# Optimization experiments

Measured on AMD Instinct MI355X. Metric: run time of the kernel, lower is better.

## Reference

```python
import jax, jax.numpy as jnp
import numpy as np

HIDDEN = 2048
HEADS = 16
HEAD_DIM = HIDDEN // HEADS  # 128
MLA_DIM = max(HEAD_DIM // 4, 8)  # 32
WINDOW = 512
B, S = 4, 2048


def setup_inputs() -> dict:
    key = jax.random.key(0)
    ks = jax.random.split(key, 9)
    sc = 0.02
    return {
        "x": jax.random.normal(ks[0], (B, S, HIDDEN), jnp.float32),
        "wq": jax.random.normal(ks[1], (HIDDEN, HIDDEN), jnp.float32) * sc,
        "wk": jax.random.normal(ks[2], (HEAD_DIM, HIDDEN), jnp.float32) * sc,
        "wv": jax.random.normal(ks[3], (HEAD_DIM, HIDDEN), jnp.float32) * sc,
        "wo": jax.random.normal(ks[4], (HIDDEN, HIDDEN), jnp.float32) * sc,
        "k_compress_w": jax.random.normal(ks[5], (MLA_DIM, HEAD_DIM), jnp.float32) * sc,
        "v_compress_w": jax.random.normal(ks[6], (MLA_DIM, HEAD_DIM), jnp.float32) * sc,
        "k_decompress_w": jax.random.normal(ks[7], (HEAD_DIM, MLA_DIM), jnp.float32) * sc,
        "v_decompress_w": jax.random.normal(ks[8], (HEAD_DIM, MLA_DIM), jnp.float32) * sc,
    }


def _rope_tables(seq_len, dim):
    inv_freq = 1.0 / (10000.0 ** (jnp.arange(0, dim, 2, dtype=jnp.float32) / dim))
    t = jnp.arange(seq_len, dtype=jnp.float32)
    freqs = jnp.outer(t, inv_freq)            # [S, dim/2]
    emb = jnp.concatenate([freqs, freqs], -1)  # [S, dim]
    return jnp.cos(emb), jnp.sin(emb)


def _rotate_half(x):
    h = x.shape[-1] // 2
    return jnp.concatenate([-x[..., h:], x[..., :h]], axis=-1)


def _quant_dequant_8bit(t):
    # global min/max 8-bit fake-quant (round has zero grad, matching uint8 detach)
    t_min, t_max = t.min(), t.max()
    scale = (t_max - t_min) / 255.0
    q = jnp.clip(jnp.round((t - t_min) / scale), 0.0, 255.0)
    return q * scale + t_min


def _swat(scores):
    attn = jax.nn.sigmoid(scores)
    return attn / (attn.sum(axis=-1, keepdims=True) + 1e-8)


def reference(x, wq, wk, wv, wo, k_compress_w, v_compress_w, k_decompress_w, v_decompress_w):
    b, s, _ = x.shape
    scale = 1.0 / np.sqrt(HEAD_DIM)

    Q = (x @ wq.T).reshape(b, s, HEADS, HEAD_DIM).transpose(0, 2, 1, 3)  # [B,H,S,D]
    K = (x @ wk.T)[:, None]  # [B,1,S,D] (single shared KV head, MQA)
    V = (x @ wv.T)[:, None]

    # RoPE (cos/sin broadcast over batch and heads)
    cos, sin = _rope_tables(s, HEAD_DIM)
    Q = Q * cos + _rotate_half(Q) * sin
    K = K * cos + _rotate_half(K) * sin

    # MLA compress -> decompress (low-rank)
    K = (K @ k_compress_w.T) @ k_decompress_w.T
    V = (V @ v_compress_w.T) @ v_decompress_w.T

    # 8-bit fake quantization
    K = _quant_dequant_8bit(K)
    V = _quant_dequant_8bit(V)

    # Sliding-window SWAT attention with linear blending of overlaps
    step = WINDOW // 2
    out = jnp.zeros_like(Q)
    for i in range(0, s, step):
        e = min(i + WINDOW, s)
        Qw = Q[:, :, i:e]           # [B,H,w,D]
        Kw = K[:, :, i:e]           # [B,1,w,D]
        Vw = V[:, :, i:e]
        scores = jnp.matmul(Qw, Kw.swapaxes(-2, -1)) * scale  # [B,H,w,w]
        wout = jnp.matmul(_swat(scores), Vw)                   # [B,H,w,D]
        if i == 0:
            out = out.at[:, :, i:e].set(wout)
        else:
            ov = min(step, e - i)
            alpha = jnp.linspace(0.0, 1.0, ov).reshape(1, 1, -1, 1)
            blended = (1 - alpha) * out[:, :, i:i + ov] + alpha * wout[:, :, :ov]
            out = out.at[:, :, i:i + ov].set(blended)
            if i + ov < e:
                out = out.at[:, :, i + ov:e].set(wout[:, :, ov:])

    out = out.transpose(0, 2, 1, 3).reshape(b, s, HIDDEN)
    return out @ wo.T
```

## Files before the change

### kernel.cpp

```cpp
#include <hip/hip_runtime.h>
#include <hip/hip_bf16.h>
#include <hip/hip_fp16.h>
#include <math.h>

#define BB 4
#define SS 2048
#define HIDDEN 2048
#define NHEADS 16
#define HDIM 128
#define BSROWS (BB * SS)
#define ATT_SCALE 0.08838834764831845f

typedef __attribute__((ext_vector_type(8))) _Float16 half8v;
typedef __attribute__((ext_vector_type(4))) float f32x4;
typedef __attribute__((ext_vector_type(16))) float f32x16;

static __device__ __forceinline__ unsigned encf(float x) {
  unsigned b = __float_as_uint(x);
  return (b & 0x80000000u) ? ~b : (b | 0x80000000u);
}
static __device__ __forceinline__ float decf(unsigned k) {
  unsigned b = (k & 0x80000000u) ? (k ^ 0x80000000u) : ~k;
  return __uint_as_float(b);
}
static __device__ __forceinline__ unsigned short f2h(float f) {
  _Float16 h = (_Float16)f;
  return *(unsigned short*)&h;
}


__global__ void rope_tables_k(float* __restrict__ ct, float* __restrict__ st) {
  int t = blockIdx.x;
  int d = threadIdx.x;
  float inv = powf(10000.0f, -(float)d * (1.0f / 64.0f));
  float a = (float)t * inv;
  ct[t * 64 + d] = cosf(a);
  st[t * 64 + d] = sinf(a);
}

__global__ void build_m_k(const float* __restrict__ kc, const float* __restrict__ kdw,
                          const float* __restrict__ vc, const float* __restrict__ vdw,
                          float* __restrict__ mk, float* __restrict__ mv) {
  int a = blockIdx.x;
  int c = threadIdx.x;
  const float* cw = blockIdx.y ? vc : kc;
  const float* dw = blockIdx.y ? vdw : kdw;
  float* m = blockIdx.y ? mv : mk;
  float acc = 0.f;
#pragma unroll
  for (int mm = 0; mm < 32; mm++) acc += cw[mm * 128 + a] * dw[c * 32 + mm];
  m[a * 128 + c] = acc;
}

__global__ void mm_init_k(unsigned* mmx) {
  int i = threadIdx.x;
  if (i < 4) mmx[i] = (i & 1) ? 0u : 0xFFFFFFFFu;
}

__global__ void split_fp16_k(const float* __restrict__ src,
                             unsigned short* __restrict__ hi, int n4) {
  int i = blockIdx.x * 256 + threadIdx.x;
  int stride = gridDim.x * 256;
  for (; i < n4; i += stride) {
    float4 v = ((const float4*)src)[i];
    ((ushort4*)hi)[i] = make_ushort4(f2h(v.x), f2h(v.y), f2h(v.z), f2h(v.w));
  }
}

__global__ __launch_bounds__(512, 2) void gemm_f16_ph_k(
    const unsigned short* __restrict__ A, const unsigned short* __restrict__ B,
    float* __restrict__ C, int NBX) {
  __shared__ unsigned short As[2][256 * 64];
  __shared__ unsigned short Bs[2][256 * 64];
  const int K = 2048;
  const int nsteps = 32;
  int tid = threadIdx.x;
  int lane = tid & 63;
  int wid = tid >> 6;
  int wm = wid >> 2, wn = wid & 3;
  int l31 = lane & 31, lg2 = lane >> 5;
  int swz = (l31 & 7) << 4;

  int nwg = gridDim.x;
  int cpx = nwg >> 3;
  int sbid = ((int)blockIdx.x & 7) * cpx + ((int)blockIdx.x >> 3);
  int by = sbid / NBX, bx = sbid % NBX;
  int m0 = by * 256, n0 = bx * 256;

  f32x16 acc[4][2] = {};

#define STAGE_A_HALF(tt_, h_, sl_)                                                 \
  do {                                                                             \
    int k0a_ = (tt_) << 6;                                                         \
    _Pragma("unroll") for (int j_ = 0; j_ < 2; ++j_) {                             \
      int L_ = j_ * 8192 + tid * 16;                                               \
      int hr_ = L_ >> 7;                                                           \
      int r_ = (hr_ & 63) + ((hr_ & 64) << 1) + (h_) * 64;                         \
      int cb_ = (L_ & 127) ^ ((r_ & 7) << 4);                                      \
      __builtin_amdgcn_global_load_lds(                                            \
          (const __attribute__((address_space(1))) void*)(A +                      \
              (size_t)(m0 + r_) * K + k0a_ + (cb_ >> 1)),                          \
          (__attribute__((address_space(3))) void*)((char*)&As[sl_][0] +           \
              (h_) * 8192 + j_ * 16384 + tid * 16), 16, 0, 0);                     \
    }                                                                              \
  } while (0)

#define STAGE_B_HALF(tt_, h_, sl_)                                                 \
  do {                                                                             \
    int k0b_ = (tt_) << 6;                                                         \
    _Pragma("unroll") for (int j_ = 0; j_ < 2; ++j_) {                             \
      int L_ = j_ * 8192 + tid * 16;                                               \
      int hr_ = L_ >> 7;                                                           \
      int r_ = (hr_ & 63) + ((hr_ & 64) << 1) + (h_) * 64;                         \
      int cb_ = (L_ & 127) ^ ((r_ & 7) << 4);                                      \
      __builtin_amdgcn_global_load_lds(                                            \
          (const __attribute__((address_space(1))) void*)(B +                      \
              (size_t)(n0 + r_) * K + k0b_ + (cb_ >> 1)),                          \
          (__attribute__((address_space(3))) void*)((char*)&Bs[sl_][0] +           \
              (h_) * 8192 + j_ * 16384 + tid * 16), 16, 0, 0);                     \
    }                                                                              \
  } while (0)

  STAGE_A_HALF(0, 0, 0);
  STAGE_A_HALF(0, 1, 0);
  STAGE_B_HALF(0, 0, 0);
  STAGE_B_HALF(0, 1, 0);
  STAGE_A_HALF(1, 0, 1);
  asm volatile("s_waitcnt vmcnt(2)" ::: "memory");
  __builtin_amdgcn_sched_barrier(0);
  __builtin_amdgcn_s_barrier();

  for (int t = 0; t < nsteps; ++t) {
    int s = t & 1;
    const char* Ab = (const char*)&As[s][0];
    const char* Bb = (const char*)&Bs[s][0];
    half8v afr[2][4], bfr[2][4];
#pragma unroll
    for (int ks = 0; ks < 4; ++ks) {
      int cb = (ks * 32 + lg2 * 16) ^ swz;
      afr[0][ks] = *(const half8v*)(Ab + (wm * 128 + 0 + l31) * 128 + cb);
      afr[1][ks] = *(const half8v*)(Ab + (wm * 128 + 32 + l31) * 128 + cb);
      bfr[0][ks] = *(const half8v*)(Bb + (wn * 64 + 0 + l31) * 128 + cb);
      bfr[1][ks] = *(const half8v*)(Bb + (wn * 64 + 32 + l31) * 128 + cb);
    }
    if (t < nsteps - 1) {
      STAGE_A_HALF(t + 1, 1, s ^ 1);
      STAGE_B_HALF(t + 1, 0, s ^ 1);
      STAGE_B_HALF(t + 1, 1, s ^ 1);
    }
    __builtin_amdgcn_s_barrier();
    asm volatile("s_waitcnt lgkmcnt(0)" ::: "memory");
    __builtin_amdgcn_sched_barrier(0);
    __builtin_amdgcn_s_setprio(1);
#pragma unroll
    for (int ks = 0; ks < 4; ++ks) {
      acc[0][0] = __builtin_amdgcn_mfma_f32_32x32x16_f16(afr[0][ks], bfr[0][ks], acc[0][0], 0, 0, 0);
      acc[0][1] = __builtin_amdgcn_mfma_f32_32x32x16_f16(afr[0][ks], bfr[1][ks], acc[0][1], 0, 0, 0);
      acc[1][0] = __builtin_amdgcn_mfma_f32_32x32x16_f16(afr[1][ks], bfr[0][ks], acc[1][0], 0, 0, 0);
      acc[1][1] = __builtin_amdgcn_mfma_f32_32x32x16_f16(afr[1][ks], bfr[1][ks], acc[1][1], 0, 0, 0);
    }
    __builtin_amdgcn_s_setprio(0);
    __builtin_amdgcn_s_barrier();
#pragma unroll
    for (int ks = 0; ks < 4; ++ks) {
      int cb = (ks * 32 + lg2 * 16) ^ swz;
      afr[0][ks] = *(const half8v*)(Ab + (wm * 128 + 64 + l31) * 128 + cb);
      afr[1][ks] = *(const half8v*)(Ab + (wm * 128 + 96 + l31) * 128 + cb);
    }
    if (t < nsteps - 2)
      STAGE_A_HALF(t + 2, 0, s);
    __builtin_amdgcn_s_barrier();
    asm volatile("s_waitcnt lgkmcnt(0)" ::: "memory");
    __builtin_amdgcn_sched_barrier(0);
    __builtin_amdgcn_s_setprio(1);
#pragma unroll
    for (int ks = 0; ks < 4; ++ks) {
      acc[2][0] = __builtin_amdgcn_mfma_f32_32x32x16_f16(afr[0][ks], bfr[0][ks], acc[2][0], 0, 0, 0);
      acc[2][1] = __builtin_amdgcn_mfma_f32_32x32x16_f16(afr[0][ks], bfr[1][ks], acc[2][1], 0, 0, 0);
      acc[3][0] = __builtin_amdgcn_mfma_f32_32x32x16_f16(afr[1][ks], bfr[0][ks], acc[3][0], 0, 0, 0);
      acc[3][1] = __builtin_amdgcn_mfma_f32_32x32x16_f16(afr[1][ks], bfr[1][ks], acc[3][1], 0, 0, 0);
    }
    __builtin_amdgcn_s_setprio(0);
    if (t < nsteps - 2)
      asm volatile("s_waitcnt vmcnt(2)" ::: "memory");
    else
      asm volatile("s_waitcnt vmcnt(0)" ::: "memory");
    __builtin_amdgcn_sched_barrier(0);
    __builtin_amdgcn_s_barrier();
  }
#undef STAGE_A_HALF
#undef STAGE_B_HALF

#pragma unroll
  for (int mi = 0; mi < 4; ++mi) {
#pragma unroll
    for (int ni = 0; ni < 2; ++ni) {
      int col = n0 + wn * 64 + ni * 32 + l31;
#pragma unroll
      for (int r = 0; r < 16; ++r) {
        int row = m0 + wm * 128 + mi * 32 + (r & 3) + 8 * (r >> 2) + 4 * lg2;
        C[(size_t)row * 2048 + col] = acc[mi][ni][r];
      }
    }
  }
}

__global__ __launch_bounds__(256) void gemm_f16_kv_k(
    const unsigned short* __restrict__ A, const unsigned short* __restrict__ B,
    float* __restrict__ Ckv) {
  const int K = 2048;
  __shared__ unsigned short As[128 * 64];
  __shared__ unsigned short Bs[128 * 64];
  int tid = threadIdx.x;
  int lane = tid & 63, wid = tid >> 6;
  int wr = wid >> 1, wc = wid & 1;
  int m0 = blockIdx.y * 128, n0 = blockIdx.x * 128;

  f32x4 acc[4][4] = {};

  int off_ = (wid << 10) + (lane << 4);
  int l15 = lane & 15, lk = lane >> 4;

  for (int t = 0; t < 32; ++t) {
    int k0 = t << 6;
    __syncthreads();
#pragma unroll
    for (int c = 0; c < 4; ++c) {
      int off = off_ + (c << 12);
      int row = off >> 7;
      int cole = (off & 127) >> 1;
      const unsigned short* ga = A + (size_t)(m0 + row) * K + k0 + cole;
      const unsigned short* gb = B + (size_t)(n0 + row) * K + k0 + cole;
      __builtin_amdgcn_global_load_lds(
          (const __attribute__((address_space(1))) void*)ga,
          (__attribute__((address_space(3))) void*)((char*)As + off), 16, 0, 0);
      __builtin_amdgcn_global_load_lds(
          (const __attribute__((address_space(1))) void*)gb,
          (__attribute__((address_space(3))) void*)((char*)Bs + off), 16, 0, 0);
    }
    __syncthreads();
#pragma unroll
    for (int ks = 0; ks < 2; ++ks) {
      half8v af[4], bf[4];
#pragma unroll
      for (int f = 0; f < 4; ++f) {
        int arow = wr * 64 + f * 16 + l15;
        int brow = wc * 64 + f * 16 + l15;
        int colb = ks * 64 + lk * 16;
        af[f] = *(const half8v*)((const char*)As + arow * 128 + colb);
        bf[f] = *(const half8v*)((const char*)Bs + brow * 128 + colb);
      }
#pragma unroll
      for (int fm = 0; fm < 4; ++fm)
#pragma unroll
        for (int fn = 0; fn < 4; ++fn)
          acc[fm][fn] = __builtin_amdgcn_mfma_f32_16x16x32_f16(af[fm], bf[fn], acc[fm][fn], 0, 0, 0);
    }
  }
#pragma unroll
  for (int fm = 0; fm < 4; ++fm) {
#pragma unroll
    for (int j = 0; j < 4; ++j) {
      int row = m0 + wr * 64 + fm * 16 + lk * 4 + j;
#pragma unroll
      for (int fn = 0; fn < 4; ++fn) {
        int col = n0 + wc * 64 + fn * 16 + l15;
        Ckv[(size_t)row * 256 + col] = acc[fm][fn][j];
      }
    }
  }
}

__global__ __launch_bounds__(128) void kv_transform_k(float* kvb,
                                                      const float* __restrict__ mk,
                                                      const float* __restrict__ mv,
                                                      const float* __restrict__ ct,
                                                      const float* __restrict__ st,
                                                      unsigned* mmx) {
  int which = blockIdx.y;
  float* base = kvb + which * 128;
  const float* M = which ? mv : mk;
  __shared__ float rowb[128];
  __shared__ float red[128];
  int tid = threadIdx.x;
  int j = tid & 63;
  float vmin = 3.4e38f, vmax = -3.4e38f;
  int r0 = blockIdx.x * 64;
  for (int ri = 0; ri < 64; ri++) {
    size_t row = r0 + ri;
    __syncthreads();
    if (which == 0) {
      int t = (int)(row & (SS - 1));
      float c = ct[t * 64 + j], s = st[t * 64 + j];
      float x0 = base[row * 256 + j];
      float x1 = base[row * 256 + j + 64];
      rowb[tid] = (tid < 64) ? (x0 * c - x1 * s) : (x1 * c + x0 * s);
    } else {
      rowb[tid] = base[row * 256 + tid];
    }
    __syncthreads();
    float acc = 0.f;
#pragma unroll 8
    for (int a = 0; a < 128; a++) acc += rowb[a] * M[a * 128 + tid];
    base[row * 256 + tid] = acc;
    vmin = fminf(vmin, acc);
    vmax = fmaxf(vmax, acc);
  }
  red[tid] = vmin;
  __syncthreads();
  for (int s2 = 64; s2 > 0; s2 >>= 1) {
    if (tid < s2) red[tid] = fminf(red[tid], red[tid + s2]);
    __syncthreads();
  }
  if (tid == 0) atomicMin(&mmx[which * 2 + 0], encf(red[0]));
  __syncthreads();
  red[tid] = vmax;
  __syncthreads();
  for (int s2 = 64; s2 > 0; s2 >>= 1) {
    if (tid < s2) red[tid] = fmaxf(red[tid], red[tid + s2]);
    __syncthreads();
  }
  if (tid == 0) atomicMax(&mmx[which * 2 + 1], encf(red[0]));
}

__global__ void quant_k_codes_k(const float* __restrict__ kvb,
                                unsigned short* __restrict__ qkc,
                                const unsigned* __restrict__ mmx) {
  int i = blockIdx.x * 256 + threadIdx.x;
  float mn = decf(mmx[0]);
  float sc = (decf(mmx[1]) - mn) * (1.f / 255.f);
  int row = i >> 7, d = i & 127;
  float v = kvb[(size_t)row * 256 + d];
  float qv = fminf(fmaxf(rintf((v - mn) / sc), 0.f), 255.f);
  qkc[i] = f2h(qv);
}

__global__ __launch_bounds__(256) void quant_vt_k(const float* __restrict__ kvb,
                                                  unsigned short* __restrict__ qvtc,
                                                  const unsigned* __restrict__ mmx) {
  int b = blockIdx.y;
  int s0 = blockIdx.x * 64;
  __shared__ unsigned short tile[128 * 72];
  float mn = decf(mmx[2]);
  float sc = (decf(mmx[3]) - mn) * (1.f / 255.f);
  for (int i = threadIdx.x; i < 8192; i += 256) {
    int sl = i >> 7, d = i & 127;
    float v = kvb[((size_t)(b * SS + s0 + sl)) * 256 + 128 + d];
    float qv = fminf(fmaxf(rintf((v - mn) / sc), 0.f), 255.f);
    tile[d * 72 + sl] = f2h(qv);
  }
  __syncthreads();
  int d = threadIdx.x >> 1, hf = threadIdx.x & 1;
  unsigned short* dst = qvtc + (size_t)(b * 128 + d) * 2048 + s0 + hf * 32;
  const unsigned short* srcp = &tile[d * 72 + hf * 32];
#pragma unroll
  for (int u = 0; u < 4; ++u)
    *(ushort4*)(dst + u * 8) = *(const ushort4*)(srcp + u * 8),
    *(ushort4*)(dst + u * 8 + 4) = *(const ushort4*)(srcp + u * 8 + 4);
}

__global__ __launch_bounds__(256, 3) void attn_mfma_k(
    const float* __restrict__ qbuf, const unsigned short* __restrict__ qkc,
    const unsigned short* __restrict__ qvtc, const unsigned* __restrict__ mmx,
    const float* __restrict__ ct, const float* __restrict__ st,
    unsigned short* __restrict__ outp) {
  __shared__ unsigned short Ks[64 * 128];
  __shared__ unsigned short Vt[128 * 64];
  __shared__ unsigned short Pl[64 * 64];
  __shared__ float sumQs[64];
  int tid = threadIdx.x;
  int lane = tid & 63, w = tid >> 6;
  int l15 = lane & 15, lg = lane >> 4;
  int swk = (l15 & 7) << 4;
  int b = blockIdx.y >> 4, h = blockIdx.y & 15;
  int t0 = blockIdx.x * 64;
  int wa = t0 >> 8;

  float mnk = decf(mmx[0]), sck = (decf(mmx[1]) - mnk) * (1.f / 255.f);
  float mnv = decf(mmx[2]), scv = (decf(mmx[3]) - mnv) * (1.f / 255.f);
  float aK = ATT_SCALE * sck;

  half8v qf[4];
  float cj[4];
  {
    int trow = t0 + w * 16 + l15;
    const float* qrow = qbuf + ((size_t)(b * SS + trow) * NHEADS + h) * HDIM + lg * 8;
    const float* cbp = ct + (size_t)trow * 64 + lg * 8;
    const float* sbp = st + (size_t)trow * 64 + lg * 8;
    float sq = 0.f;
#pragma unroll
    for (int half = 0; half < 2; ++half) {
      float4 xa = *(const float4*)(qrow + half * 32);
      float4 xb = *(const float4*)(qrow + half * 32 + 4);
      float4 ya = *(const float4*)(qrow + half * 32 + 64);
      float4 yb = *(const float4*)(qrow + half * 32 + 68);
      float4 ca = *(const float4*)(cbp + half * 32);
      float4 cb4 = *(const float4*)(cbp + half * 32 + 4);
      float4 sa = *(const float4*)(sbp + half * 32);
      float4 sb4 = *(const float4*)(sbp + half * 32 + 4);
      float xv[8] = {xa.x, xa.y, xa.z, xa.w, xb.x, xb.y, xb.z, xb.w};
      float yv[8] = {ya.x, ya.y, ya.z, ya.w, yb.x, yb.y, yb.z, yb.w};
      float cv[8] = {ca.x, ca.y, ca.z, ca.w, cb4.x, cb4.y, cb4.z, cb4.w};
      float sv[8] = {sa.x, sa.y, sa.z, sa.w, sb4.x, sb4.y, sb4.z, sb4.w};
      half8v tlo, thi;
#pragma unroll
      for (int u = 0; u < 8; ++u) {
        float r0 = xv[u] * cv[u] - yv[u] * sv[u];
        float r1 = yv[u] * cv[u] + xv[u] * sv[u];
        sq += r0 + r1;
        tlo[u] = (_Float16)r0;
        thi[u] = (_Float16)r1;
      }
      qf[half] = tlo;
      qf[half + 2] = thi;
      __builtin_amdgcn_sched_barrier(0);
    }
    sq += __shfl_xor(sq, 16);
    sq += __shfl_xor(sq, 32);
    if (lane < 16) sumQs[w * 16 + l15] = sq;
#pragma unroll
    for (int j = 0; j < 4; ++j) cj[j] = ATT_SCALE * mnk * sumQs[w * 16 + lg * 4 + j];
  }

  f32x4 zz = {0.f, 0.f, 0.f, 0.f};
  f32x4 acc0[8], acc1[8];
#pragma unroll
  for (int i = 0; i < 8; ++i) { acc0[i] = zz; acc1[i] = zz; }
  float rs0[4] = {0, 0, 0, 0}, rs1[4] = {0, 0, 0, 0};
  int base = wa * 256;

  int n = (wa == 0 || wa == 7) ? 8 : 12;
  int segoff = (wa == 0) ? 1 : 0;
  int kbase = (wa == 0) ? base : base - 256;

#define STAGE_K(K0)                                                                \
  do {                                                                             \
    int k0_ = (K0);                                                                \
    const char* kb_ = (const char*)qkc + ((size_t)b * SS + k0_) * 256;             \
    _Pragma("unroll") for (int i_ = 0; i_ < 4; ++i_) {                             \
      int L_ = w * 4096 + i_ * 1024 + lane * 16;                                   \
      int kr_ = L_ >> 8;                                                           \
      int kd_ = (L_ & 255) ^ ((kr_ & 7) << 4);                                     \
      __builtin_amdgcn_global_load_lds(                                            \
          (const __attribute__((address_space(1))) void*)(kb_ + kr_ * 256 + kd_),  \
          (__attribute__((address_space(3))) void*)((char*)Ks + L_), 16, 0, 0);    \
    }                                                                              \
  } while (0)

#define STAGE_V(K0)                                                                \
  do {                                                                             \
    int k0_ = (K0);                                                                \
    const char* vb_ = (const char*)qvtc + (size_t)b * 524288 + (size_t)k0_ * 2;    \
    _Pragma("unroll") for (int i_ = 0; i_ < 4; ++i_) {                             \
      int L_ = w * 4096 + i_ * 1024 + lane * 16;                                   \
      int vr_ = L_ >> 7;                                                           \
      int vd_ = (L_ & 127) ^ ((vr_ & 7) << 4);                                     \
      __builtin_amdgcn_global_load_lds(                                            \
          (const __attribute__((address_space(1))) void*)(vb_ + vr_ * 4096 + vd_), \
          (__attribute__((address_space(3))) void*)((char*)Vt + L_), 16, 0, 0);    \
    }                                                                              \
  } while (0)

  STAGE_K(kbase);
  STAGE_V(kbase);
  asm volatile("s_waitcnt vmcnt(4)" ::: "memory");
  __builtin_amdgcn_sched_barrier(0);
  __builtin_amdgcn_s_barrier();

  for (int i = 0; i < n; ++i) {
    int sg = segoff + (i >> 2);
    bool d0 = (sg <= 1) && (wa > 0);
    bool d1 = (sg >= 1);
    {
      f32x4 sf0 = zz, sf1 = zz, sf2 = zz, sf3 = zz;
#pragma unroll
      for (int kk = 0; kk < 4; ++kk) {
        int cb = (kk * 64 + lg * 16) ^ swk;
        half8v k0f = *(const half8v*)((const char*)Ks + (0 * 16 + l15) * 256 + cb);
        half8v k1f = *(const half8v*)((const char*)Ks + (1 * 16 + l15) * 256 + cb);
        half8v k2f = *(const half8v*)((const char*)Ks + (2 * 16 + l15) * 256 + cb);
        half8v k3f = *(const half8v*)((const char*)Ks + (3 * 16 + l15) * 256 + cb);
        sf0 = __builtin_amdgcn_mfma_f32_16x16x32_f16(qf[kk], k0f, sf0, 0, 0, 0);
        sf1 = __builtin_amdgcn_mfma_f32_16x16x32_f16(qf[kk], k1f, sf1, 0, 0, 0);
        sf2 = __builtin_amdgcn_mfma_f32_16x16x32_f16(qf[kk], k2f, sf2, 0, 0, 0);
        sf3 = __builtin_amdgcn_mfma_f32_16x16x32_f16(qf[kk], k3f, sf3, 0, 0, 0);
      }
      float rsc[4] = {0.f, 0.f, 0.f, 0.f};
#pragma unroll
      for (int nf = 0; nf < 4; ++nf) {
        f32x4 sv = (nf == 0) ? sf0 : (nf == 1) ? sf1 : (nf == 2) ? sf2 : sf3;
#pragma unroll
        for (int j = 0; j < 4; ++j) {
          float s_ = aK * sv[j] + cj[j];
          float p_ = 1.f / (1.f + __expf(-s_));
          rsc[j] += p_;
          int prow = w * 16 + lg * 4 + j;
          int paddr = prow * 128 + (((nf * 16 + l15) * 2) ^ ((prow & 7) << 4));
          *(unsigned short*)((char*)Pl + paddr) = f2h(p_);
        }
      }
#pragma unroll
      for (int j = 0; j < 4; ++j) {
        rsc[j] += __shfl_xor(rsc[j], 1);
        rsc[j] += __shfl_xor(rsc[j], 2);
        rsc[j] += __shfl_xor(rsc[j], 4);
        rsc[j] += __shfl_xor(rsc[j], 8);
        if (d0) rs0[j] += rsc[j];
        if (d1) rs1[j] += rsc[j];
      }
    }
    __builtin_amdgcn_s_barrier();
    if (i + 1 < n) {
      STAGE_K(kbase + (i + 1) * 64);
      asm volatile("s_waitcnt vmcnt(4)" ::: "memory");
    } else {
      asm volatile("s_waitcnt vmcnt(0)" ::: "memory");
    }
    __builtin_amdgcn_sched_barrier(0);
    __builtin_amdgcn_s_barrier();
    {
      half8v pf0, pf1;
      int prow = w * 16 + l15;
      pf0 = *(const half8v*)((const char*)Pl + prow * 128 + ((lg * 16) ^ swk));
      pf1 = *(const half8v*)((const char*)Pl + prow * 128 + ((64 + lg * 16) ^ swk));
#pragma unroll
      for (int nf = 0; nf < 8; ++nf) {
        int vb0 = (nf * 16 + l15) * 128 + ((lg * 16) ^ swk);
        int vb1 = (nf * 16 + l15) * 128 + ((64 + lg * 16) ^ swk);
        half8v vf0 = *(const half8v*)((const char*)Vt + vb0);
        half8v vf1 = *(const half8v*)((const char*)Vt + vb1);
        if (d0) {
          acc0[nf] = __builtin_amdgcn_mfma_f32_16x16x32_f16(pf0, vf0, acc0[nf], 0, 0, 0);
          acc0[nf] = __builtin_amdgcn_mfma_f32_16x16x32_f16(pf1, vf1, acc0[nf], 0, 0, 0);
        }
        if (d1) {
          acc1[nf] = __builtin_amdgcn_mfma_f32_16x16x32_f16(pf0, vf0, acc1[nf], 0, 0, 0);
          acc1[nf] = __builtin_amdgcn_mfma_f32_16x16x32_f16(pf1, vf1, acc1[nf], 0, 0, 0);
        }
      }
    }
    __builtin_amdgcn_s_barrier();
    if (i + 1 < n) {
      STAGE_V(kbase + (i + 1) * 64);
      asm volatile("s_waitcnt vmcnt(4)" ::: "memory");
      __builtin_amdgcn_sched_barrier(0);
      __builtin_amdgcn_s_barrier();
    }
  }
#undef STAGE_K
#undef STAGE_V

#pragma unroll
  for (int j = 0; j < 4; ++j) {
    int t = t0 + w * 16 + lg * 4 + j;
    float al = (float)(t & 255) * (1.f / 255.f);
    float r0 = rs0[j], r1 = rs1[j];
    float i0 = 1.f / (r0 + 1e-8f), i1 = 1.f / (r1 + 1e-8f);
    float w0 = (wa == 0) ? 0.f : (1.f - al);
    float w1 = (wa == 0) ? 1.f : al;
    size_t obase = ((size_t)(b * SS + t) * NHEADS + h) * HDIM;
#pragma unroll
    for (int nf = 0; nf < 8; ++nf) {
      float o0 = (scv * acc0[nf][j] + mnv * r0) * i0;
      float o1 = (scv * acc1[nf][j] + mnv * r1) * i1;
      outp[obase + nf * 16 + l15] = f2h(w0 * o0 + w1 * o1);
    }
  }
}

extern "C" void kernel_launch(void* const* d_in, const int* in_sizes, int n_in,
                              void* d_out, int out_size, void* d_ws, size_t ws_size,
                              hipStream_t stream) {
  const float* x = (const float*)d_in[0];
  const float* wq = (const float*)d_in[1];
  const float* wk = (const float*)d_in[2];
  const float* wv = (const float*)d_in[3];
  const float* wo = (const float*)d_in[4];
  const float* kcw = (const float*)d_in[5];
  const float* vcw = (const float*)d_in[6];
  const float* kdw = (const float*)d_in[7];
  const float* vdw = (const float*)d_in[8];
  float* out = (float*)d_out;

  const size_t QN = (size_t)BSROWS * HIDDEN;
  const size_t KVN = (size_t)BSROWS * 256;

  float* q = (float*)d_ws;
  float* kvb = q + QN;
  float* ct = kvb + KVN;
  float* st = ct + SS * 64;
  float* mk = st + SS * 64;
  float* mv = mk + 128 * 128;
  unsigned* mmx = (unsigned*)(mv + 128 * 128);
  unsigned short* xh = (unsigned short*)(mmx + 16);
  unsigned short* wqkvh = xh + QN;
  unsigned short* woh = wqkvh + (size_t)2304 * 2048;
  unsigned short* qkc = woh + (size_t)HIDDEN * HIDDEN;
  unsigned short* qvtc = qkc + (size_t)BSROWS * 128;

  rope_tables_k<<<SS, 64, 0, stream>>>(ct, st);
  build_m_k<<<dim3(128, 2), 128, 0, stream>>>(kcw, kdw, vcw, vdw, mk, mv);

  split_fp16_k<<<2048, 256, 0, stream>>>(x, xh, (int)(QN / 4));
  split_fp16_k<<<512, 256, 0, stream>>>(wq, wqkvh, HIDDEN * HIDDEN / 4);
  split_fp16_k<<<256, 256, 0, stream>>>(wk, wqkvh + (size_t)2048 * 2048, HDIM * HIDDEN / 4);
  split_fp16_k<<<256, 256, 0, stream>>>(wv, wqkvh + (size_t)2176 * 2048, HDIM * HIDDEN / 4);
  split_fp16_k<<<512, 256, 0, stream>>>(wo, woh, HIDDEN * HIDDEN / 4);

  gemm_f16_kv_k<<<dim3(2, 64), 256, 0, stream>>>(xh, wqkvh + (size_t)2048 * 2048, kvb);
  gemm_f16_ph_k<<<256, 512, 0, stream>>>(xh, wqkvh, q, 8);

  mm_init_k<<<1, 64, 0, stream>>>(mmx);
  kv_transform_k<<<dim3(BSROWS / 64, 2), 128, 0, stream>>>(kvb, mk, mv, ct, st, mmx);
  quant_k_codes_k<<<(BSROWS * 128) / 256, 256, 0, stream>>>(kvb, qkc, mmx);
  quant_vt_k<<<dim3(SS / 64, BB), 256, 0, stream>>>(kvb, qvtc, mmx);

  attn_mfma_k<<<dim3(SS / 64, BB * NHEADS), 256, 0, stream>>>(q, qkc, qvtc, mmx, ct, st,
                                                              xh);

  gemm_f16_ph_k<<<256, 512, 0, stream>>>(xh, woh, out, 8);
}
```

Baseline: 594.5 us.

## Store Q projection in fp16, restage GEMM prefetch, widen kv_transform blocks

The Q projection GEMM now writes fp16 instead of fp32, and the attention kernel reads half8 vectors and converts them before RoPE. This halves Q write and read traffic at the cost of rounding Q to fp16 before RoPE rather than after. The GEMM pipeline is reorganised to issue the whole next-stage A/B prefetch at the top of each iteration with new wait counts, replacing the split prefetch across two stages. kv_transform moves to 256 threads that each handle two rows per iteration, to raise parallelism.

```diff
diff --git a/kernel.cpp b/kernel.cpp
--- a/kernel.cpp
+++ b/kernel.cpp
@@ -69,7 +69,7 @@
 
 __global__ __launch_bounds__(512, 2) void gemm_f16_ph_k(
     const unsigned short* __restrict__ A, const unsigned short* __restrict__ B,
-    float* __restrict__ C, int NBX) {
+    float* __restrict__ Cf, unsigned short* __restrict__ Ch, int NBX) {
   __shared__ unsigned short As[2][256 * 64];
   __shared__ unsigned short Bs[2][256 * 64];
   const int K = 2048;
@@ -122,11 +122,10 @@
   } while (0)
 
   STAGE_A_HALF(0, 0, 0);
-  STAGE_A_HALF(0, 1, 0);
   STAGE_B_HALF(0, 0, 0);
   STAGE_B_HALF(0, 1, 0);
-  STAGE_A_HALF(1, 0, 1);
-  asm volatile("s_waitcnt vmcnt(2)" ::: "memory");
+  STAGE_A_HALF(0, 1, 0);
+  asm volatile("s_waitcnt vmcnt(0)" ::: "memory");
   __builtin_amdgcn_sched_barrier(0);
   __builtin_amdgcn_s_barrier();
 
@@ -135,6 +134,12 @@
     const char* Ab = (const char*)&As[s][0];
     const char* Bb = (const char*)&Bs[s][0];
     half8v afr[2][4], bfr[2][4];
+    if (t + 1 < nsteps) {
+      STAGE_A_HALF(t + 1, 0, s ^ 1);
+      STAGE_B_HALF(t + 1, 0, s ^ 1);
+      STAGE_B_HALF(t + 1, 1, s ^ 1);
+      STAGE_A_HALF(t + 1, 1, s ^ 1);
+    }
 #pragma unroll
     for (int ks = 0; ks < 4; ++ks) {
       int cb = (ks * 32 + lg2 * 16) ^ swz;
@@ -143,11 +148,6 @@
       bfr[0][ks] = *(const half8v*)(Bb + (wn * 64 + 0 + l31) * 128 + cb);
       bfr[1][ks] = *(const half8v*)(Bb + (wn * 64 + 32 + l31) * 128 + cb);
     }
-    if (t < nsteps - 1) {
-      STAGE_A_HALF(t + 1, 1, s ^ 1);
-      STAGE_B_HALF(t + 1, 0, s ^ 1);
-      STAGE_B_HALF(t + 1, 1, s ^ 1);
-    }
     __builtin_amdgcn_s_barrier();
     asm volatile("s_waitcnt lgkmcnt(0)" ::: "memory");
     __builtin_amdgcn_sched_barrier(0);
@@ -160,6 +160,11 @@
       acc[1][1] = __builtin_amdgcn_mfma_f32_32x32x16_f16(afr[1][ks], bfr[1][ks], acc[1][1], 0, 0, 0);
     }
     __builtin_amdgcn_s_setprio(0);
+    if (t + 1 < nsteps)
+      asm volatile("s_waitcnt vmcnt(8)" ::: "memory");
+    else
+      asm volatile("s_waitcnt vmcnt(0)" ::: "memory");
+    __builtin_amdgcn_sched_barrier(0);
     __builtin_amdgcn_s_barrier();
 #pragma unroll
     for (int ks = 0; ks < 4; ++ks) {
@@ -167,8 +172,6 @@
       afr[0][ks] = *(const half8v*)(Ab + (wm * 128 + 64 + l31) * 128 + cb);
       afr[1][ks] = *(const half8v*)(Ab + (wm * 128 + 96 + l31) * 128 + cb);
     }
-    if (t < nsteps - 2)
-      STAGE_A_HALF(t + 2, 0, s);
     __builtin_amdgcn_s_barrier();
     asm volatile("s_waitcnt lgkmcnt(0)" ::: "memory");
     __builtin_amdgcn_sched_barrier(0);
@@ -181,7 +184,7 @@
       acc[3][1] = __builtin_amdgcn_mfma_f32_32x32x16_f16(afr[1][ks], bfr[1][ks], acc[3][1], 0, 0, 0);
     }
     __builtin_amdgcn_s_setprio(0);
-    if (t < nsteps - 2)
+    if (t + 1 < nsteps)
       asm volatile("s_waitcnt vmcnt(2)" ::: "memory");
     else
       asm volatile("s_waitcnt vmcnt(0)" ::: "memory");
@@ -199,7 +202,11 @@
 #pragma unroll
       for (int r = 0; r < 16; ++r) {
         int row = m0 + wm * 128 + mi * 32 + (r & 3) + 8 * (r >> 2) + 4 * lg2;
-        C[(size_t)row * 2048 + col] = acc[mi][ni][r];
+        float v = acc[mi][ni][r];
+        if (Ch)
+          Ch[(size_t)row * 2048 + col] = f2h(v);
+        else
+          Cf[(size_t)row * 2048 + col] = v;
       }
     }
   }
@@ -271,7 +278,7 @@
   }
 }
 
-__global__ __launch_bounds__(128) void kv_transform_k(float* kvb,
+__global__ __launch_bounds__(256) void kv_transform_k(float* kvb,
                                                       const float* __restrict__ mk,
                                                       const float* __restrict__ mv,
                                                       const float* __restrict__ ct,
@@ -280,35 +287,37 @@
   int which = blockIdx.y;
   float* base = kvb + which * 128;
   const float* M = which ? mv : mk;
-  __shared__ float rowb[128];
-  __shared__ float red[128];
+  __shared__ float rowb[256];
+  __shared__ float red[256];
   int tid = threadIdx.x;
-  int j = tid & 63;
+  int half = tid >> 7, col = tid & 127;
   float vmin = 3.4e38f, vmax = -3.4e38f;
   int r0 = blockIdx.x * 64;
-  for (int ri = 0; ri < 64; ri++) {
-    size_t row = r0 + ri;
+  for (int ri = 0; ri < 32; ri++) {
+    size_t row = r0 + ri * 2 + half;
     __syncthreads();
     if (which == 0) {
       int t = (int)(row & (SS - 1));
+      int j = col & 63;
       float c = ct[t * 64 + j], s = st[t * 64 + j];
       float x0 = base[row * 256 + j];
       float x1 = base[row * 256 + j + 64];
-      rowb[tid] = (tid < 64) ? (x0 * c - x1 * s) : (x1 * c + x0 * s);
+      rowb[tid] = (col < 64) ? (x0 * c - x1 * s) : (x1 * c + x0 * s);
     } else {
-      rowb[tid] = base[row * 256 + tid];
+      rowb[tid] = base[row * 256 + col];
     }
     __syncthreads();
     float acc = 0.f;
+    const float* rb = &rowb[half * 128];
 #pragma unroll 8
-    for (int a = 0; a < 128; a++) acc += rowb[a] * M[a * 128 + tid];
-    base[row * 256 + tid] = acc;
+    for (int a = 0; a < 128; a++) acc += rb[a] * M[a * 128 + col];
+    base[row * 256 + col] = acc;
     vmin = fminf(vmin, acc);
     vmax = fmaxf(vmax, acc);
   }
   red[tid] = vmin;
   __syncthreads();
-  for (int s2 = 64; s2 > 0; s2 >>= 1) {
+  for (int s2 = 128; s2 > 0; s2 >>= 1) {
     if (tid < s2) red[tid] = fminf(red[tid], red[tid + s2]);
     __syncthreads();
   }
@@ -316,7 +325,7 @@
   __syncthreads();
   red[tid] = vmax;
   __syncthreads();
-  for (int s2 = 64; s2 > 0; s2 >>= 1) {
+  for (int s2 = 128; s2 > 0; s2 >>= 1) {
     if (tid < s2) red[tid] = fmaxf(red[tid], red[tid + s2]);
     __syncthreads();
   }
@@ -360,7 +369,7 @@
 }
 
 __global__ __launch_bounds__(256, 3) void attn_mfma_k(
-    const float* __restrict__ qbuf, const unsigned short* __restrict__ qkc,
+    const unsigned short* __restrict__ qh, const unsigned short* __restrict__ qkc,
     const unsigned short* __restrict__ qvtc, const unsigned* __restrict__ mmx,
     const float* __restrict__ ct, const float* __restrict__ st,
     unsigned short* __restrict__ outp) {
@@ -384,29 +393,27 @@
   float cj[4];
   {
     int trow = t0 + w * 16 + l15;
-    const float* qrow = qbuf + ((size_t)(b * SS + trow) * NHEADS + h) * HDIM + lg * 8;
+    const unsigned short* qrow =
+        qh + ((size_t)(b * SS + trow) * NHEADS + h) * HDIM + lg * 8;
     const float* cbp = ct + (size_t)trow * 64 + lg * 8;
     const float* sbp = st + (size_t)trow * 64 + lg * 8;
     float sq = 0.f;
 #pragma unroll
     for (int half = 0; half < 2; ++half) {
-      float4 xa = *(const float4*)(qrow + half * 32);
-      float4 xb = *(const float4*)(qrow + half * 32 + 4);
-      float4 ya = *(const float4*)(qrow + half * 32 + 64);
-      float4 yb = *(const float4*)(qrow + half * 32 + 68);
+      half8v xa8 = *(const half8v*)(qrow + half * 32);
+      half8v ya8 = *(const half8v*)(qrow + half * 32 + 64);
       float4 ca = *(const float4*)(cbp + half * 32);
       float4 cb4 = *(const float4*)(cbp + half * 32 + 4);
       float4 sa = *(const float4*)(sbp + half * 32);
       float4 sb4 = *(const float4*)(sbp + half * 32 + 4);
-      float xv[8] = {xa.x, xa.y, xa.z, xa.w, xb.x, xb.y, xb.z, xb.w};
-      float yv[8] = {ya.x, ya.y, ya.z, ya.w, yb.x, yb.y, yb.z, yb.w};
       float cv[8] = {ca.x, ca.y, ca.z, ca.w, cb4.x, cb4.y, cb4.z, cb4.w};
       float sv[8] = {sa.x, sa.y, sa.z, sa.w, sb4.x, sb4.y, sb4.z, sb4.w};
       half8v tlo, thi;
 #pragma unroll
       for (int u = 0; u < 8; ++u) {
-        float r0 = xv[u] * cv[u] - yv[u] * sv[u];
-        float r1 = yv[u] * cv[u] + xv[u] * sv[u];
+        float xv = (float)xa8[u], yv = (float)ya8[u];
+        float r0 = xv * cv[u] - yv * sv[u];
+        float r1 = yv * cv[u] + xv * sv[u];
         sq += r0 + r1;
         tlo[u] = (_Float16)r0;
         thi[u] = (_Float16)r1;
@@ -585,8 +592,8 @@
   const size_t QN = (size_t)BSROWS * HIDDEN;
   const size_t KVN = (size_t)BSROWS * 256;
 
-  float* q = (float*)d_ws;
-  float* kvb = q + QN;
+  unsigned short* qh = (unsigned short*)d_ws;
+  float* kvb = (float*)(qh + QN);
   float* ct = kvb + KVN;
   float* st = ct + SS * 64;
   float* mk = st + SS * 64;
@@ -608,15 +615,15 @@
   split_fp16_k<<<512, 256, 0, stream>>>(wo, woh, HIDDEN * HIDDEN / 4);
 
   gemm_f16_kv_k<<<dim3(2, 64), 256, 0, stream>>>(xh, wqkvh + (size_t)2048 * 2048, kvb);
-  gemm_f16_ph_k<<<256, 512, 0, stream>>>(xh, wqkvh, q, 8);
+  gemm_f16_ph_k<<<256, 512, 0, stream>>>(xh, wqkvh, nullptr, qh, 8);
 
   mm_init_k<<<1, 64, 0, stream>>>(mmx);
-  kv_transform_k<<<dim3(BSROWS / 64, 2), 128, 0, stream>>>(kvb, mk, mv, ct, st, mmx);
+  kv_transform_k<<<dim3(BSROWS / 64, 2), 256, 0, stream>>>(kvb, mk, mv, ct, st, mmx);
   quant_k_codes_k<<<(BSROWS * 128) / 256, 256, 0, stream>>>(kvb, qkc, mmx);
   quant_vt_k<<<dim3(SS / 64, BB), 256, 0, stream>>>(kvb, qvtc, mmx);
 
-  attn_mfma_k<<<dim3(SS / 64, BB * NHEADS), 256, 0, stream>>>(q, qkc, qvtc, mmx, ct, st,
+  attn_mfma_k<<<dim3(SS / 64, BB * NHEADS), 256, 0, stream>>>(qh, qkc, qvtc, mmx, ct, st,
                                                               xh);
 
-  gemm_f16_ph_k<<<256, 512, 0, stream>>>(xh, woh, out, 8);
-}
+  gemm_f16_ph_k<<<256, 512, 0, stream>>>(xh, woh, out, nullptr, 8);
+}
```

Result: faster. 555.9 us (-6.5%).
